# Performance work log

Measured on AMD Instinct MI355X. Metric: run time of the kernel, lower is better.

Reference implementation:

```python
import jax, jax.numpy as jnp
import numpy as np

B, T, D = 4, 8192, 1024
N_PROTO = 8


def setup_inputs() -> dict:
    key = jax.random.key(0)
    k1, k2, k3 = jax.random.split(key, 3)
    x = jax.random.normal(k1, (B, T, D), dtype=jnp.float32)
    # torch Linear kaiming-uniform scale ~ 1/sqrt(fan_in); keeps tanh unsaturated
    W = jax.random.normal(k2, (6, D), dtype=jnp.float32) * (1.0 / np.sqrt(D))
    prototypes = jax.random.normal(k3, (N_PROTO, 6), dtype=jnp.float32)
    hamming_scale = jnp.float32(0.1)
    return {"x": x, "W": W, "prototypes": prototypes, "hamming_scale": hamming_scale}


def reference(x, W, prototypes, hamming_scale):
    # q6_project: tanh(Linear(x)) then L2-normalize with clamp(min=1e-6)
    z = jnp.tanh(jnp.einsum('btd,kd->btk', x, W))            # (B,T,6)
    z = z / jnp.clip(jnp.linalg.norm(z, axis=-1, keepdims=True), 1e-6)
    # F.normalize(prototypes, dim=-1) with eps=1e-12
    p = prototypes / jnp.clip(jnp.linalg.norm(prototypes, axis=-1, keepdims=True), 1e-12)
    dot = jnp.einsum('btk,pk->btp', z, p)                    # (B,T,P)
    dist = (6.0 - dot * 6.0) * 0.5                            # Theorem-3 Hamming distance
    return jax.nn.softmax(-hamming_scale * dist, axis=-1)    # routing weights (B,T,P)
```

## Files before the change

### kernel.cpp

```cpp
#include <hip/hip_runtime.h>


#define DIM 1024
#define NK 6
#define NPROTO 8
#define TPI 4

__global__ __launch_bounds__(256, 2) void q6_fused_kernel(
    const float* __restrict__ x,
    const float* __restrict__ W,
    const float* __restrict__ protos,
    const float* __restrict__ hs_ptr,
    float* __restrict__ out,
    int n_tokens, int n_waves)
{
    const int lane = threadIdx.x & 63;
    const int wave_id = blockIdx.x * (blockDim.x >> 6) + (threadIdx.x >> 6);
    const int cbase = lane * 4;

    float4 wreg[NK][4];
#pragma unroll
    for (int k = 0; k < NK; ++k)
#pragma unroll
        for (int j = 0; j < 4; ++j)
            wreg[k][j] = *reinterpret_cast<const float4*>(&W[k * DIM + j * 256 + cbase]);

    const int pl = lane & 7;
    float p[NK];
#pragma unroll
    for (int k = 0; k < NK; ++k) p[k] = protos[pl * NK + k];
    {
        float pn = sqrtf(p[0]*p[0] + p[1]*p[1] + p[2]*p[2] + p[3]*p[3] + p[4]*p[4] + p[5]*p[5]);
        float inv = 1.0f / fmaxf(pn, 1e-12f);
#pragma unroll
        for (int k = 0; k < NK; ++k) p[k] *= inv;
    }
    const float hs = hs_ptr[0];

    const bool hi5 = (lane & 32) != 0;
    const bool hi4 = (lane & 16) != 0;
    const int tloc = lane >> 4;
    const int pidx = lane & 15;

    for (int tb = wave_id * TPI; tb < n_tokens; tb += n_waves * TPI) {
        float4 xv[TPI][4];
#pragma unroll
        for (int t = 0; t < TPI; ++t) {
            const float* xt = x + (size_t)(tb + t) * DIM;
#pragma unroll
            for (int j = 0; j < 4; ++j)
                xv[t][j] = *reinterpret_cast<const float4*>(&xt[j * 256 + cbase]);
        }

        float acc[TPI][NK];
#pragma unroll
        for (int t = 0; t < TPI; ++t)
#pragma unroll
            for (int k = 0; k < NK; ++k) acc[t][k] = 0.0f;
#pragma unroll
        for (int t = 0; t < TPI; ++t)
#pragma unroll
            for (int j = 0; j < 4; ++j) {
                const float4 xvj = xv[t][j];
#pragma unroll
                for (int k = 0; k < NK; ++k) {
                    float a = acc[t][k];
                    a = fmaf(xvj.x, wreg[k][j].x, a);
                    a = fmaf(xvj.y, wreg[k][j].y, a);
                    a = fmaf(xvj.z, wreg[k][j].z, a);
                    a = fmaf(xvj.w, wreg[k][j].w, a);
                    acc[t][k] = a;
                }
            }

        float r[2][NK];
#pragma unroll
        for (int tp = 0; tp < 2; ++tp)
#pragma unroll
            for (int k = 0; k < NK; ++k) {
                float send = hi5 ? acc[tp][k]     : acc[2 + tp][k];
                float keep = hi5 ? acc[2 + tp][k] : acc[tp][k];
                r[tp][k] = keep + __shfl_xor(send, 32, 64);
            }

        float z[NK];
#pragma unroll
        for (int k = 0; k < NK; ++k) {
            float send = hi4 ? r[0][k] : r[1][k];
            float keep = hi4 ? r[1][k] : r[0][k];
            z[k] = keep + __shfl_xor(send, 16, 64);
        }

#pragma unroll
        for (int off = 8; off >= 1; off >>= 1)
#pragma unroll
            for (int k = 0; k < NK; ++k)
                z[k] += __shfl_xor(z[k], off, 64);

        if (pidx < NPROTO) {
            float zz[NK];
            float nrm2 = 0.0f;
#pragma unroll
            for (int k = 0; k < NK; ++k) {
                float a = z[k];
                float e = __expf(-2.0f * fabsf(a));
                float th = (1.0f - e) / (1.0f + e);
                zz[k] = copysignf(th, a);
                nrm2 = fmaf(zz[k], zz[k], nrm2);
            }
            float inv = 1.0f / fmaxf(sqrtf(nrm2), 1e-6f);
            float dot = (zz[0]*p[0] + zz[1]*p[1] + zz[2]*p[2] +
                         zz[3]*p[3] + zz[4]*p[4] + zz[5]*p[5]) * inv;
            float logit = -hs * (6.0f - dot * 6.0f) * 0.5f;
            float m = logit;
            m = fmaxf(m, __shfl_xor(m, 1, 64));
            m = fmaxf(m, __shfl_xor(m, 2, 64));
            m = fmaxf(m, __shfl_xor(m, 4, 64));
            float e = __expf(logit - m);
            float s = e;
            s += __shfl_xor(s, 1, 64);
            s += __shfl_xor(s, 2, 64);
            s += __shfl_xor(s, 4, 64);
            out[(size_t)(tb + tloc) * NPROTO + pidx] = e / s;
        }
    }
}

extern "C" void kernel_launch(void* const* d_in, const int* in_sizes, int n_in,
                              void* d_out, int out_size, void* d_ws, size_t ws_size,
                              hipStream_t stream) {
    const float* x      = (const float*)d_in[0];
    const float* W      = (const float*)d_in[1];
    const float* protos = (const float*)d_in[2];
    const float* hs     = (const float*)d_in[3];
    float* out = (float*)d_out;

    const int n_tokens = in_sizes[0] / DIM;
    const int blocks = 2048;
    const int threads = 256;
    const int n_waves = blocks * (threads / 64);

    q6_fused_kernel<<<blocks, threads, 0, stream>>>(
        x, W, protos, hs, out, n_tokens, n_waves);
}
```

Measured before the change: 192.1 us.

## Double-buffer token loads with fixed per-wave chunks of contiguous tokens

Result: slower. 196.5 us (+2.3%).

```diff
diff --git a/kernel.cpp b/kernel.cpp
--- a/kernel.cpp
+++ b/kernel.cpp
@@ -4,7 +4,8 @@
 #define DIM 1024
 #define NK 6
 #define NPROTO 8
-#define TPI 4
+#define TPI 2
+#define ITERS 8
 
 __global__ __launch_bounds__(256, 2) void q6_fused_kernel(
     const float* __restrict__ x,
@@ -12,7 +13,7 @@
     const float* __restrict__ protos,
     const float* __restrict__ hs_ptr,
     float* __restrict__ out,
-    int n_tokens, int n_waves)
+    int n_tokens)
 {
     const int lane = threadIdx.x & 63;
     const int wave_id = blockIdx.x * (blockDim.x >> 6) + (threadIdx.x >> 6);
@@ -38,18 +39,34 @@
     const float hs = hs_ptr[0];
 
     const bool hi5 = (lane & 32) != 0;
-    const bool hi4 = (lane & 16) != 0;
-    const int tloc = lane >> 4;
-    const int pidx = lane & 15;
+    const int tloc = lane >> 5;
+    const int pidx = lane & 31;
 
-    for (int tb = wave_id * TPI; tb < n_tokens; tb += n_waves * TPI) {
-        float4 xv[TPI][4];
+    const int tok0 = wave_id * (TPI * ITERS);
+    if (tok0 >= n_tokens) return;
+
+    float4 xbuf[2][TPI][4];
+#pragma unroll
+    for (int t = 0; t < TPI; ++t) {
+        const float* xt = x + (size_t)(tok0 + t) * DIM;
+#pragma unroll
+        for (int j = 0; j < 4; ++j)
+            xbuf[0][t][j] = *reinterpret_cast<const float4*>(&xt[j * 256 + cbase]);
+    }
+
+#pragma unroll 2
+    for (int i = 0; i < ITERS; ++i) {
+        const int cur = i & 1;
+        const int tb = tok0 + i * TPI;
+
+        int nb = tb + TPI;
+        if (nb > n_tokens - TPI) nb = n_tokens - TPI;
 #pragma unroll
         for (int t = 0; t < TPI; ++t) {
-            const float* xt = x + (size_t)(tb + t) * DIM;
+            const float* xt = x + (size_t)(nb + t) * DIM;
 #pragma unroll
             for (int j = 0; j < 4; ++j)
-                xv[t][j] = *reinterpret_cast<const float4*>(&xt[j * 256 + cbase]);
+                xbuf[cur ^ 1][t][j] = *reinterpret_cast<const float4*>(&xt[j * 256 + cbase]);
         }
 
         float acc[TPI][NK];
@@ -61,7 +78,7 @@
         for (int t = 0; t < TPI; ++t)
 #pragma unroll
             for (int j = 0; j < 4; ++j) {
-                const float4 xvj = xv[t][j];
+                const float4 xvj = xbuf[cur][t][j];
 #pragma unroll
                 for (int k = 0; k < NK; ++k) {
                     float a = acc[t][k];
@@ -73,26 +90,15 @@
                 }
             }
 
-        float r[2][NK];
-#pragma unroll
-        for (int tp = 0; tp < 2; ++tp)
-#pragma unroll
-            for (int k = 0; k < NK; ++k) {
-                float send = hi5 ? acc[tp][k]     : acc[2 + tp][k];
-                float keep = hi5 ? acc[2 + tp][k] : acc[tp][k];
-                r[tp][k] = keep + __shfl_xor(send, 32, 64);
-            }
-
         float z[NK];
 #pragma unroll
         for (int k = 0; k < NK; ++k) {
-            float send = hi4 ? r[0][k] : r[1][k];
-            float keep = hi4 ? r[1][k] : r[0][k];
-            z[k] = keep + __shfl_xor(send, 16, 64);
+            float send = hi5 ? acc[0][k] : acc[1][k];
+            float keep = hi5 ? acc[1][k] : acc[0][k];
+            z[k] = keep + __shfl_xor(send, 32, 64);
         }
-
 #pragma unroll
-        for (int off = 8; off >= 1; off >>= 1)
+        for (int off = 16; off >= 1; off >>= 1)
 #pragma unroll
             for (int k = 0; k < NK; ++k)
                 z[k] += __shfl_xor(z[k], off, 64);
@@ -136,10 +142,9 @@
     float* out = (float*)d_out;
 
     const int n_tokens = in_sizes[0] / DIM;
-    const int blocks = 2048;
+    const int blocks = 512;
     const int threads = 256;
-    const int n_waves = blocks * (threads / 64);
 
     q6_fused_kernel<<<blocks, threads, 0, stream>>>(
-        x, W, protos, hs, out, n_tokens, n_waves);
+        x, W, protos, hs, out, n_tokens);
 }
```
